# Kernel tuning notes

Hardware: AMD Instinct MI355X
Metric: run time of the kernel (lower is better)

Reference implementation:

```python
import jax, jax.numpy as jnp
import numpy as np

EMBED_DIM = 1024
HEAD_NUM = 16
HEAD_DIM = EMBED_DIM // HEAD_NUM
T, B, S = 2048, 4, 2048


def setup_inputs() -> dict:
    key = jax.random.key(0)
    ks = jax.random.split(key, 11)
    s = 0.02
    return {
        "query": jax.random.normal(ks[0], (T, B, EMBED_DIM), jnp.float32),
        "key": jax.random.normal(ks[1], (S, B, EMBED_DIM), jnp.float32),
        "value": jax.random.normal(ks[2], (S, B, EMBED_DIM), jnp.float32),
        "q_proj_weight": jax.random.normal(ks[3], (EMBED_DIM, EMBED_DIM), jnp.float32) * s,
        "k_proj_weight": jax.random.normal(ks[4], (EMBED_DIM, EMBED_DIM), jnp.float32) * s,
        "v_proj_weight": jax.random.normal(ks[5], (EMBED_DIM, EMBED_DIM), jnp.float32) * s,
        "in_proj_bias": jax.random.normal(ks[6], (3 * EMBED_DIM,), jnp.float32) * s,
        "bias_k": jax.random.normal(ks[7], (1, 1, EMBED_DIM), jnp.float32) * s,
        "bias_v": jax.random.normal(ks[8], (1, 1, EMBED_DIM), jnp.float32) * s,
        "out_proj_weight": jax.random.normal(ks[9], (EMBED_DIM, EMBED_DIM), jnp.float32) * s,
        "out_proj_bias": jax.random.normal(ks[10], (EMBED_DIM,), jnp.float32) * s,
    }


def reference(query, key, value, q_proj_weight, k_proj_weight, v_proj_weight,
              in_proj_bias, bias_k, bias_v, out_proj_weight, out_proj_bias):
    t, b, e = query.shape
    h, hd = HEAD_NUM, HEAD_DIM
    scaling = float(hd) ** -0.5
    # input projections (F.linear: x @ W.T + b)
    q = (query @ q_proj_weight.T + in_proj_bias[:e]) * scaling          # [T,B,E]
    k = key @ k_proj_weight.T + in_proj_bias[e:2 * e]                   # [S,B,E]
    v = value @ v_proj_weight.T + in_proj_bias[2 * e:]                  # [S,B,E]
    # append bias_k / bias_v token along the sequence dim
    k = jnp.concatenate([k, jnp.broadcast_to(bias_k, (1, b, e))], axis=0)  # [S+1,B,E]
    v = jnp.concatenate([v, jnp.broadcast_to(bias_v, (1, b, e))], axis=0)  # [S+1,B,E]
    # split heads: [L, B, E] -> [B*H, L, hd]
    q = q.reshape(t, b * h, hd).transpose(1, 0, 2)
    k = k.reshape(-1, b * h, hd).transpose(1, 0, 2)
    v = v.reshape(-1, b * h, hd).transpose(1, 0, 2)
    # full O(T*S) attention, as in the original bmm->softmax->bmm
    weights = jax.nn.softmax(jnp.einsum('nqd,nkd->nqk', q, k), axis=-1)  # [B*H,T,S+1]
    out = jnp.einsum('nqk,nkd->nqd', weights, v)                         # [B*H,T,hd]
    out = out.transpose(1, 0, 2).reshape(t, b, e)
    out = out @ out_proj_weight.T + out_proj_bias
    avg_weights = weights.sum(axis=1) / h                                # [B*H,S+1]
    return out, avg_weights
```

## Files before the change

### kernel.cpp

```cpp
#include <hip/hip_runtime.h>

#define T_DIM 2048
#define B_DIM 4
#define S_DIM 2048
#define E_DIM 1024
#define H_NUM 16
#define HD    64
#define NH    64
#define SP1   2049
#define SPAD  2112
#define NCHUNK 33

typedef short bf16x8 __attribute__((ext_vector_type(8)));
typedef short bf16x4 __attribute__((ext_vector_type(4)));
typedef float f32x4  __attribute__((ext_vector_type(4)));
typedef float f32x16 __attribute__((ext_vector_type(16)));
typedef unsigned int u32;

#define QSCALE 0.18033688011112042f

#if __has_builtin(__builtin_amdgcn_exp2f)
__device__ __forceinline__ float exp2_fast(float x) { return __builtin_amdgcn_exp2f(x); }
#else
__device__ __forceinline__ float exp2_fast(float x) { return __expf(x * 0.6931471805599453f); }
#endif

__device__ __forceinline__ unsigned short f2bf(float x) {
    union { float f; unsigned int u; } v; v.f = x;
    unsigned int r = v.u + 0x7FFFu + ((v.u >> 16) & 1u);
    return (unsigned short)(r >> 16);
}

__device__ __forceinline__ u32 cvtpk_bf16(float lo, float hi) {
    u32 r;
    asm("v_cvt_pk_bf16_f32 %0, %1, %2" : "=v"(r) : "v"(lo), "v"(hi));
    return r;
}
__device__ __forceinline__ void plswap(u32& a, u32& b) {
    asm("v_permlane32_swap_b32 %0, %1" : "+v"(a), "+v"(b));
}

__global__ __launch_bounds__(256)
void cvt_w4(const float* __restrict__ w0, const float* __restrict__ w1,
            const float* __restrict__ w2, const float* __restrict__ w3,
            short* __restrict__ dst)
{
    const int y = blockIdx.y;
    const float* src = (y == 0) ? w0 : (y == 1) ? w1 : (y == 2) ? w2 : w3;
    short* d = dst + (size_t)y * E_DIM * E_DIM;
    const int i = blockIdx.x * 256 + threadIdx.x;
    const float4* s = reinterpret_cast<const float4*>(src) + (size_t)i * 2;
    float4 a = s[0], b = s[1];
    uint4 o;
    o.x = cvtpk_bf16(a.x, a.y); o.y = cvtpk_bf16(a.z, a.w);
    o.z = cvtpk_bf16(b.x, b.y); o.w = cvtpk_bf16(b.z, b.w);
    *(reinterpret_cast<uint4*>(d) + i) = o;
}

template<int MODE>
__global__ __launch_bounds__(256)
void gemm_bf16(const void* __restrict__ Xq, const void* __restrict__ Xk,
               const void* __restrict__ Xv, const short* __restrict__ Wall,
               const float* __restrict__ biasAll, void* __restrict__ outp)
{
    __shared__ short As[128][72];
    __shared__ short Bs[128][72];
    const int bm = blockIdx.x, bn = blockIdx.y;
    const int z = (MODE == 0) ? blockIdx.z : 0;
    const void* Ap = (MODE == 3) ? Xq : (z == 0) ? Xq : (z == 1) ? Xk : Xv;
    const short* W = Wall + (size_t)z * E_DIM * E_DIM;
    const float* bias = biasAll + z * E_DIM;

    const int tid = threadIdx.x;
    const int l = tid & 63, w = tid >> 6;
    const int wr = w >> 1, wc = w & 1;
    const int lr = l & 15, lg = l >> 4;
    const int rb = tid >> 3, cg = tid & 7;

    float4 paA[4], paB[4];
    bf16x8 pa3[4];
    bf16x8 pb[4];

    auto load_tiles = [&](int k0) {
#pragma unroll
        for (int it = 0; it < 4; ++it) {
            const int row = it * 32 + rb;
            if (MODE == 3) {
                const int m = bm * 128 + row;
                const size_t asrc =
                    ((size_t)((m & 3) * 16 + (k0 >> 6)) * T_DIM + (m >> 2)) * HD + cg * 8;
                pa3[it] = *reinterpret_cast<const bf16x8*>((const short*)Ap + asrc);
            } else {
                const float* ap = (const float*)Ap + (size_t)(bm * 128 + row) * E_DIM + k0 + cg * 8;
                paA[it] = *reinterpret_cast<const float4*>(ap);
                paB[it] = *reinterpret_cast<const float4*>(ap + 4);
            }
            pb[it] = *reinterpret_cast<const bf16x8*>(
                W + (size_t)(bn * 128 + row) * E_DIM + k0 + cg * 8);
        }
    };
    auto write_tiles = [&]() {
#pragma unroll
        for (int it = 0; it < 4; ++it) {
            const int row = it * 32 + rb;
            if (MODE == 3) {
                *reinterpret_cast<bf16x8*>(&As[row][cg * 8]) = pa3[it];
            } else {
                uint4 st;
                st.x = cvtpk_bf16(paA[it].x, paA[it].y); st.y = cvtpk_bf16(paA[it].z, paA[it].w);
                st.z = cvtpk_bf16(paB[it].x, paB[it].y); st.w = cvtpk_bf16(paB[it].z, paB[it].w);
                *reinterpret_cast<uint4*>(&As[row][cg * 8]) = st;
            }
            *reinterpret_cast<bf16x8*>(&Bs[row][cg * 8]) = pb[it];
        }
    };

    load_tiles(0);
    write_tiles();
    __syncthreads();

    f32x4 acc[4][4] = {};

    for (int k0 = 0; k0 < E_DIM; k0 += 64) {
        const bool more = (k0 + 64 < E_DIM);
        if (more) load_tiles(k0 + 64);

        __builtin_amdgcn_s_setprio(1);
#pragma unroll
        for (int c = 0; c < 2; ++c) {
            bf16x8 af[4], bf[4];
#pragma unroll
            for (int mi = 0; mi < 4; ++mi)
                af[mi] = *reinterpret_cast<const bf16x8*>(&As[wr * 64 + mi * 16 + lr][c * 32 + lg * 8]);
#pragma unroll
            for (int ni = 0; ni < 4; ++ni)
                bf[ni] = *reinterpret_cast<const bf16x8*>(&Bs[wc * 64 + ni * 16 + lr][c * 32 + lg * 8]);
#pragma unroll
            for (int mi = 0; mi < 4; ++mi)
#pragma unroll
                for (int ni = 0; ni < 4; ++ni)
                    acc[mi][ni] = __builtin_amdgcn_mfma_f32_16x16x32_bf16(
                        af[mi], bf[ni], acc[mi][ni], 0, 0, 0);
        }
        __builtin_amdgcn_s_setprio(0);

        if (more) {
            __syncthreads();
            write_tiles();
            __syncthreads();
        }
    }

#pragma unroll
    for (int mi = 0; mi < 4; ++mi)
#pragma unroll
        for (int ni = 0; ni < 4; ++ni) {
            const int colg = bn * 128 + wc * 64 + ni * 16 + lr;
            const float bv = bias[colg];
#pragma unroll
            for (int r = 0; r < 4; ++r) {
                const int m = bm * 128 + wr * 64 + mi * 16 + lg * 4 + r;
                float v = acc[mi][ni][r] + bv;
                if (MODE == 3) {
                    ((float*)outp)[(size_t)m * E_DIM + colg] = v;
                } else {
                    if (z == 0) v *= QSCALE;
                    const int seq = m >> 2, b = m & 3;
                    const int head = colg >> 6, d = colg & 63;
                    const int sd = (z == 0) ? T_DIM : SPAD;
                    short* ob = (short*)outp;
                    if (z == 1) ob += (size_t)NH * T_DIM * HD;
                    else if (z == 2) ob += (size_t)NH * T_DIM * HD + (size_t)NH * SPAD * HD;
                    ob[((size_t)(b * 16 + head) * sd + seq) * HD + d] = (short)f2bf(v);
                }
            }
        }
}

__global__ void fill_kv_pad(short* __restrict__ k_h, short* __restrict__ v_h,
                            const float* __restrict__ bias_k,
                            const float* __restrict__ bias_v)
{
    const int d   = threadIdx.x;
    const int row = S_DIM + blockIdx.x;
    const int n   = blockIdx.y;
    short bk = 0, bv = 0;
    if (row == S_DIM) {
        bk = (short)f2bf(bias_k[(n & 15) * HD + d]);
        bv = (short)f2bf(bias_v[(n & 15) * HD + d]);
    }
    const size_t idx = ((size_t)n * SPAD + row) * HD + d;
    k_h[idx] = bk;
    v_h[idx] = bv;
}

__global__ __launch_bounds__(512, 4)
void attn_mfma(const short* __restrict__ q_h, const short* __restrict__ k_h,
               const short* __restrict__ v_h, short* __restrict__ o_h,
               float* __restrict__ m_arr, float* __restrict__ l_arr)
{
    __shared__ short KsD[2][64 * 64];
    __shared__ short VtD[2][64 * 64];

    const int id = blockIdx.x;
    const int xcd = id & 7, slot = id >> 3;
    const int n = xcd * 8 + (slot >> 3);
    const int q0 = (slot & 7) * 256;

    const int tid = threadIdx.x, l = tid & 63, w = tid >> 6;
    const int ql = l & 31;
    const int hi = l >> 5;
    const int qrow = q0 + w * 32 + ql;

    const int krow = tid >> 3, kcg = tid & 7;
    const int kswz = (kcg * 16) ^ ((krow & 7) << 4);
    const int sp = tid & 31, dq = tid >> 5;

    const short* kbase = k_h + (size_t)n * SPAD * HD;
    const short* vbase = v_h + (size_t)n * SPAD * HD;

    bf16x8 aq0, aq1, aq2, aq3;
    {
        const short* qp = q_h + ((size_t)n * T_DIM + qrow) * HD + hi * 8;
        aq0 = *(const bf16x8*)(qp);
        aq1 = *(const bf16x8*)(qp + 16);
        aq2 = *(const bf16x8*)(qp + 32);
        aq3 = *(const bf16x8*)(qp + 48);
    }

    bf16x8 pk  = *(const bf16x8*)(kbase + (size_t)krow * HD + kcg * 8);
    bf16x4 pva = *(const bf16x4*)(vbase + (size_t)(2 * sp) * HD + dq * 4);
    bf16x4 pvb = *(const bf16x4*)(vbase + (size_t)(2 * sp + 1) * HD + dq * 4);
    {
        char* KsB = (char*)KsD[0];
        char* VtB = (char*)VtD[0];
        *(bf16x8*)(KsB + krow * 128 + kswz) = pk;
#pragma unroll
        for (int j = 0; j < 4; ++j) {
            u32 pkd = (u32)(unsigned short)pva[j] | ((u32)(unsigned short)pvb[j] << 16);
            const int d = dq * 4 + j;
            *(u32*)(VtB + d * 128 + ((4 * sp) ^ ((d & 7) << 4))) = pkd;
        }
    }
    __syncthreads();

    float m_run = -1e30f, l_run = 0.f;
    f32x16 accA, accB;
#pragma unroll
    for (int r = 0; r < 16; ++r) { accA[r] = 0.f; accB[r] = 0.f; }

    for (int kc = 0; kc < NCHUNK; ++kc) {
        const char* KsB = (const char*)KsD[kc & 1];
        const char* VtB = (const char*)VtD[kc & 1];
        const bool more = (kc + 1 < NCHUNK);

        if (more) {
            const int s0n = (kc + 1) * 64;
            pk  = *(const bf16x8*)(kbase + (size_t)(s0n + krow) * HD + kcg * 8);
            pva = *(const bf16x4*)(vbase + (size_t)(s0n + 2 * sp) * HD + dq * 4);
            pvb = *(const bf16x4*)(vbase + (size_t)(s0n + 2 * sp + 1) * HD + dq * 4);
        }

        f32x16 sc0, sc1;
#pragma unroll
        for (int r = 0; r < 16; ++r) { sc0[r] = 0.f; sc1[r] = 0.f; }
        __builtin_amdgcn_s_setprio(1);
#pragma unroll
        for (int sl = 0; sl < 4; ++sl) {
            const int cb = ((sl * 32) + hi * 16) ^ ((ql & 7) << 4);
            bf16x8 kf0 = *(const bf16x8*)(KsB + ql * 128 + cb);
            bf16x8 kf1 = *(const bf16x8*)(KsB + (32 + ql) * 128 + cb);
            bf16x8 qf = (sl == 0) ? aq0 : (sl == 1) ? aq1 : (sl == 2) ? aq2 : aq3;
            sc0 = __builtin_amdgcn_mfma_f32_32x32x16_bf16(kf0, qf, sc0, 0, 0, 0);
            sc1 = __builtin_amdgcn_mfma_f32_32x32x16_bf16(kf1, qf, sc1, 0, 0, 0);
        }
        __builtin_amdgcn_s_setprio(0);

        const int s0 = kc * 64;
        if (s0 + 64 > SP1) {
#pragma unroll
            for (int r = 0; r < 16; ++r) {
                const int key = (r & 3) + 8 * (r >> 2) + 4 * hi;
                if (s0 + key >= SP1)      sc0[r] = -1e30f;
                if (s0 + 32 + key >= SP1) sc1[r] = -1e30f;
            }
        }

        float mv[16];
#pragma unroll
        for (int r = 0; r < 16; ++r) mv[r] = fmaxf(sc0[r], sc1[r]);
#pragma unroll
        for (int s = 8; s > 0; s >>= 1)
#pragma unroll
            for (int r = 0; r < s; ++r) mv[r] = fmaxf(mv[r], mv[r + s]);
        float mx = fmaxf(mv[0], __shfl_xor(mv[0], 32));
        if (!__all(mx - m_run <= 8.0f)) {
            const float mnew = fmaxf(m_run, mx);
            const float fac = exp2_fast(m_run - mnew);
            l_run *= fac;
#pragma unroll
            for (int r = 0; r < 16; ++r) { accA[r] *= fac; accB[r] *= fac; }
            m_run = mnew;
        }
        float p0[16], p1[16];
#pragma unroll
        for (int r = 0; r < 16; ++r) p0[r] = exp2_fast(sc0[r] - m_run);
#pragma unroll
        for (int r = 0; r < 16; ++r) p1[r] = exp2_fast(sc1[r] - m_run);
        float sv[16];
#pragma unroll
        for (int r = 0; r < 16; ++r) sv[r] = p0[r] + p1[r];
#pragma unroll
        for (int s = 8; s > 0; s >>= 1)
#pragma unroll
            for (int r = 0; r < s; ++r) sv[r] += sv[r + s];
        l_run += sv[0] + __shfl_xor(sv[0], 32);

        union PF { u32 u[4]; bf16x8 v; };
        PF pf0, pf1, pf2, pf3;
        {
            u32 a0 = cvtpk_bf16(p0[0], p0[1]),   b0 = cvtpk_bf16(p0[4], p0[5]);   plswap(a0, b0);
            u32 a1 = cvtpk_bf16(p0[2], p0[3]),   b1 = cvtpk_bf16(p0[6], p0[7]);   plswap(a1, b1);
            u32 a2 = cvtpk_bf16(p0[8], p0[9]),   b2 = cvtpk_bf16(p0[12], p0[13]); plswap(a2, b2);
            u32 a3 = cvtpk_bf16(p0[10], p0[11]), b3 = cvtpk_bf16(p0[14], p0[15]); plswap(a3, b3);
            pf0.u[0] = a0; pf0.u[1] = a1; pf0.u[2] = b0; pf0.u[3] = b1;
            pf1.u[0] = a2; pf1.u[1] = a3; pf1.u[2] = b2; pf1.u[3] = b3;
            u32 c0 = cvtpk_bf16(p1[0], p1[1]),   d0_ = cvtpk_bf16(p1[4], p1[5]);   plswap(c0, d0_);
            u32 c1 = cvtpk_bf16(p1[2], p1[3]),   d1_ = cvtpk_bf16(p1[6], p1[7]);   plswap(c1, d1_);
            u32 c2 = cvtpk_bf16(p1[8], p1[9]),   d2_ = cvtpk_bf16(p1[12], p1[13]); plswap(c2, d2_);
            u32 c3 = cvtpk_bf16(p1[10], p1[11]), d3_ = cvtpk_bf16(p1[14], p1[15]); plswap(c3, d3_);
            pf2.u[0] = c0; pf2.u[1] = c1; pf2.u[2] = d0_; pf2.u[3] = d1_;
            pf3.u[0] = c2; pf3.u[1] = c3; pf3.u[2] = d2_; pf3.u[3] = d3_;
        }

        __builtin_amdgcn_s_setprio(1);
#pragma unroll
        for (int ksl = 0; ksl < 4; ++ksl) {
            const int cb = ((ksl * 32) + hi * 16) ^ ((ql & 7) << 4);
            bf16x8 vf0 = *(const bf16x8*)(VtB + ql * 128 + cb);
            bf16x8 vf1 = *(const bf16x8*)(VtB + (32 + ql) * 128 + cb);
            const bf16x8 pv = (ksl == 0) ? pf0.v : (ksl == 1) ? pf1.v : (ksl == 2) ? pf2.v : pf3.v;
            accA = __builtin_amdgcn_mfma_f32_32x32x16_bf16(vf0, pv, accA, 0, 0, 0);
            accB = __builtin_amdgcn_mfma_f32_32x32x16_bf16(vf1, pv, accB, 0, 0, 0);
        }
        __builtin_amdgcn_s_setprio(0);

        if (more) {
            char* KsN = (char*)KsD[(kc & 1) ^ 1];
            char* VtN = (char*)VtD[(kc & 1) ^ 1];
            *(bf16x8*)(KsN + krow * 128 + kswz) = pk;
#pragma unroll
            for (int j = 0; j < 4; ++j) {
                u32 pkd = (u32)(unsigned short)pva[j] | ((u32)(unsigned short)pvb[j] << 16);
                const int d = dq * 4 + j;
                *(u32*)(VtN + d * 128 + ((4 * sp) ^ ((d & 7) << 4))) = pkd;
            }
            __syncthreads();
        }
    }

    const float il = 1.0f / l_run;
    short* orow = o_h + ((size_t)n * T_DIM + qrow) * HD;
#pragma unroll
    for (int rq = 0; rq < 4; ++rq) {
        uint2 st;
        st.x = cvtpk_bf16(accA[rq * 4 + 0] * il, accA[rq * 4 + 1] * il);
        st.y = cvtpk_bf16(accA[rq * 4 + 2] * il, accA[rq * 4 + 3] * il);
        *(uint2*)(orow + rq * 8 + hi * 4) = st;
        uint2 st2;
        st2.x = cvtpk_bf16(accB[rq * 4 + 0] * il, accB[rq * 4 + 1] * il);
        st2.y = cvtpk_bf16(accB[rq * 4 + 2] * il, accB[rq * 4 + 3] * il);
        *(uint2*)(orow + 32 + rq * 8 + hi * 4) = st2;
    }
    if (hi == 0) {
        m_arr[n * T_DIM + qrow] = m_run;
        l_arr[n * T_DIM + qrow] = l_run;
    }
}

__global__ __launch_bounds__(256)
void colsum_mfma(const short* __restrict__ q_h, const short* __restrict__ k_h,
                 const float* __restrict__ m_arr, const float* __restrict__ l_arr,
                 float* __restrict__ avg_out)
{
    __shared__ short Qs[2][64][72];
    __shared__ float msh[2][64];
    __shared__ float lih[2][64];

    const int id = blockIdx.x;
    const int xcd = id & 7, slot = id >> 3;
    const int n = xcd * 8 + slot / 33;
    const int s0 = (slot % 33) * 64;

    const int tid = threadIdx.x, l = tid & 63, w = tid >> 6;
    const int lr = l & 15, lg = l >> 4;
    const int qr = tid >> 3, qcg = tid & 7;

    const short* qbase = q_h + (size_t)n * T_DIM * HD;

    bf16x8 ak[2];
#pragma unroll
    for (int c = 0; c < 2; ++c)
        ak[c] = *reinterpret_cast<const bf16x8*>(
            k_h + ((size_t)n * SPAD + s0 + w * 16 + lr) * HD + c * 32 + lg * 8);

    bf16x8 qa = *(const bf16x8*)(qbase + (size_t)qr * HD + qcg * 8);
    bf16x8 qb = *(const bf16x8*)(qbase + (size_t)(32 + qr) * HD + qcg * 8);
    float mlv = 0.f;
    if (tid < 64) mlv = m_arr[n * T_DIM + tid];
    else if (tid < 128) mlv = l_arr[n * T_DIM + tid - 64];
    *(bf16x8*)&Qs[0][qr][qcg * 8] = qa;
    *(bf16x8*)&Qs[0][32 + qr][qcg * 8] = qb;
    if (tid < 64) msh[0][tid] = mlv;
    else if (tid < 128) lih[0][tid - 64] = 1.0f / mlv;
    __syncthreads();

    float csum[4] = {0.f, 0.f, 0.f, 0.f};

    for (int it = 0; it < T_DIM / 64; ++it) {
        const int buf = it & 1;
        const bool more = (it + 1 < T_DIM / 64);
        if (more) {
            const int qo = (it + 1) * 64;
            qa = *(const bf16x8*)(qbase + (size_t)(qo + qr) * HD + qcg * 8);
            qb = *(const bf16x8*)(qbase + (size_t)(qo + 32 + qr) * HD + qcg * 8);
            if (tid < 64) mlv = m_arr[n * T_DIM + qo + tid];
            else if (tid < 128) mlv = l_arr[n * T_DIM + qo + tid - 64];
        }
        __builtin_amdgcn_s_setprio(1);
#pragma unroll
        for (int qt = 0; qt < 4; ++qt) {
            bf16x8 bq0 = *reinterpret_cast<const bf16x8*>(&Qs[buf][qt * 16 + lr][lg * 8]);
            bf16x8 bq1 = *reinterpret_cast<const bf16x8*>(&Qs[buf][qt * 16 + lr][32 + lg * 8]);
            f32x4 z = {0.f, 0.f, 0.f, 0.f};
            z = __builtin_amdgcn_mfma_f32_16x16x32_bf16(ak[0], bq0, z, 0, 0, 0);
            z = __builtin_amdgcn_mfma_f32_16x16x32_bf16(ak[1], bq1, z, 0, 0, 0);
            const float mq = msh[buf][qt * 16 + lr];
            const float lq = lih[buf][qt * 16 + lr];
#pragma unroll
            for (int r = 0; r < 4; ++r)
                csum[r] += exp2_fast(z[r] - mq) * lq;
        }
        __builtin_amdgcn_s_setprio(0);
        if (more) {
            *(bf16x8*)&Qs[buf ^ 1][qr][qcg * 8] = qa;
            *(bf16x8*)&Qs[buf ^ 1][32 + qr][qcg * 8] = qb;
            if (tid < 64) msh[buf ^ 1][tid] = mlv;
            else if (tid < 128) lih[buf ^ 1][tid - 64] = 1.0f / mlv;
            __syncthreads();
        }
    }

#pragma unroll
    for (int r = 0; r < 4; ++r) {
        float v = csum[r];
        v += __shfl_xor(v, 1, 16);
        v += __shfl_xor(v, 2, 16);
        v += __shfl_xor(v, 4, 16);
        v += __shfl_xor(v, 8, 16);
        if (lr == 0) {
            const int key = s0 + w * 16 + lg * 4 + r;
            if (key < SP1) avg_out[(size_t)n * SP1 + key] = v * 0.0625f;
        }
    }
}

extern "C" void kernel_launch(void* const* d_in, const int* in_sizes, int n_in,
                              void* d_out, int out_size, void* d_ws, size_t ws_size,
                              hipStream_t stream)
{
    const float* query   = (const float*)d_in[0];
    const float* key     = (const float*)d_in[1];
    const float* value   = (const float*)d_in[2];
    const float* wq      = (const float*)d_in[3];
    const float* wk      = (const float*)d_in[4];
    const float* wv      = (const float*)d_in[5];
    const float* in_bias = (const float*)d_in[6];
    const float* bias_k  = (const float*)d_in[7];
    const float* bias_v  = (const float*)d_in[8];
    const float* wo      = (const float*)d_in[9];
    const float* out_b   = (const float*)d_in[10];
    float* out = (float*)d_out;

    short* wqb = (short*)d_ws;
    short* wob = wqb + (size_t)3 * E_DIM * E_DIM;
    short* q_h = wqb + (size_t)4 * E_DIM * E_DIM;
    short* k_h = q_h + (size_t)NH * T_DIM * HD;
    short* v_h = k_h + (size_t)NH * SPAD * HD;
    short* o_h = v_h + (size_t)NH * SPAD * HD;
    float* m_arr = (float*)(o_h + (size_t)NH * T_DIM * HD);
    float* l_arr = m_arr + (size_t)NH * T_DIM;

    const dim3 blk(256);
    hipLaunchKernelGGL(cvt_w4, dim3(512, 4), blk, 0, stream, wq, wk, wv, wo, wqb);

    hipLaunchKernelGGL((gemm_bf16<0>), dim3(64, 8, 3), blk, 0, stream,
                       (const void*)query, (const void*)key, (const void*)value,
                       wqb, in_bias, (void*)q_h);
    hipLaunchKernelGGL(fill_kv_pad, dim3(SPAD - S_DIM, NH), dim3(64), 0, stream,
                       k_h, v_h, bias_k, bias_v);
    hipLaunchKernelGGL(attn_mfma, dim3(512), dim3(512), 0, stream,
                       q_h, k_h, v_h, o_h, m_arr, l_arr);
    hipLaunchKernelGGL(colsum_mfma, dim3(2112), blk, 0, stream,
                       q_h, k_h, m_arr, l_arr, out + (size_t)T_DIM * B_DIM * E_DIM);
    hipLaunchKernelGGL((gemm_bf16<3>), dim3(64, 8), blk, 0, stream,
                       (const void*)o_h, (const void*)o_h, (const void*)o_h,
                       wob, out_b, (void*)out);
}
```

Baseline: 294.1 us.

## Pre-convert QKV inputs to bf16 and stage GEMM tiles via direct global-to-LDS loads

Adds a separate kernel that converts query/key/value from fp32 to bf16 into workspace, so the projection GEMM reads bf16 only. The GEMM now loads tiles with global_load_lds straight into unpadded LDS instead of going through registers. This drops the register prefetch double-buffering, removes the row padding, and sets launch bounds to 4 blocks per CU. It costs an extra full pass over the activations, leaves no overlap between loads and MFMA, and unpadded LDS rows may cause bank conflicts on fragment reads.

```diff
diff --git a/kernel.cpp b/kernel.cpp
--- a/kernel.cpp
+++ b/kernel.cpp
@@ -10,6 +10,7 @@
 #define SP1   2049
 #define SPAD  2112
 #define NCHUNK 33
+#define NTOKE ((size_t)T_DIM * B_DIM * E_DIM)
 
 typedef short bf16x8 __attribute__((ext_vector_type(8)));
 typedef short bf16x4 __attribute__((ext_vector_type(4)));
@@ -38,6 +39,12 @@
 }
 __device__ __forceinline__ void plswap(u32& a, u32& b) {
     asm("v_permlane32_swap_b32 %0, %1" : "+v"(a), "+v"(b));
+}
+
+__device__ __forceinline__ void load_lds16(const void* g, void* l) {
+    __builtin_amdgcn_global_load_lds(
+        (const __attribute__((address_space(1))) unsigned int*)g,
+        (__attribute__((address_space(3))) unsigned int*)l, 16, 0, 0);
 }
 
 __global__ __launch_bounds__(256)
@@ -57,73 +64,58 @@
     *(reinterpret_cast<uint4*>(d) + i) = o;
 }
 
+__global__ __launch_bounds__(256)
+void cvt_in(const float* __restrict__ q, const float* __restrict__ k,
+            const float* __restrict__ v, short* __restrict__ dst)
+{
+    const int y = blockIdx.y;
+    const float* src = (y == 0) ? q : (y == 1) ? k : v;
+    short* d = dst + (size_t)y * NTOKE;
+    const size_t i = (size_t)blockIdx.x * 256 + threadIdx.x;
+    const float4* s = reinterpret_cast<const float4*>(src) + i * 2;
+    float4 a = s[0], b = s[1];
+    uint4 o;
+    o.x = cvtpk_bf16(a.x, a.y); o.y = cvtpk_bf16(a.z, a.w);
+    o.z = cvtpk_bf16(b.x, b.y); o.w = cvtpk_bf16(b.z, b.w);
+    *(reinterpret_cast<uint4*>(d) + i) = o;
+}
+
 template<int MODE>
-__global__ __launch_bounds__(256)
-void gemm_bf16(const void* __restrict__ Xq, const void* __restrict__ Xk,
-               const void* __restrict__ Xv, const short* __restrict__ Wall,
+__global__ __launch_bounds__(256, 4)
+void gemm_bf16(const short* __restrict__ Abase, const short* __restrict__ Wall,
                const float* __restrict__ biasAll, void* __restrict__ outp)
 {
-    __shared__ short As[128][72];
-    __shared__ short Bs[128][72];
+    __shared__ short As[128][64];
+    __shared__ short Bs[128][64];
     const int bm = blockIdx.x, bn = blockIdx.y;
     const int z = (MODE == 0) ? blockIdx.z : 0;
-    const void* Ap = (MODE == 3) ? Xq : (z == 0) ? Xq : (z == 1) ? Xk : Xv;
-    const short* W = Wall + (size_t)z * E_DIM * E_DIM;
+    const short* Az = Abase + (MODE == 0 ? (size_t)z * NTOKE : 0);
+    const short* W  = Wall + (size_t)z * E_DIM * E_DIM;
     const float* bias = biasAll + z * E_DIM;
 
     const int tid = threadIdx.x;
     const int l = tid & 63, w = tid >> 6;
     const int wr = w >> 1, wc = w & 1;
     const int lr = l & 15, lg = l >> 4;
-    const int rb = tid >> 3, cg = tid & 7;
-
-    float4 paA[4], paB[4];
-    bf16x8 pa3[4];
-    bf16x8 pb[4];
-
-    auto load_tiles = [&](int k0) {
-#pragma unroll
-        for (int it = 0; it < 4; ++it) {
-            const int row = it * 32 + rb;
+    const int srow = tid >> 3, scol = (tid & 7) * 8;
+
+    f32x4 acc[4][4] = {};
+
+    for (int k0 = 0; k0 < E_DIM; k0 += 64) {
+#pragma unroll
+        for (int r = 0; r < 4; ++r) {
+            const int row = r * 32 + srow;
+            const short* ga;
             if (MODE == 3) {
                 const int m = bm * 128 + row;
-                const size_t asrc =
-                    ((size_t)((m & 3) * 16 + (k0 >> 6)) * T_DIM + (m >> 2)) * HD + cg * 8;
-                pa3[it] = *reinterpret_cast<const bf16x8*>((const short*)Ap + asrc);
+                ga = Az + ((size_t)((m & 3) * 16 + (k0 >> 6)) * T_DIM + (m >> 2)) * HD + scol;
             } else {
-                const float* ap = (const float*)Ap + (size_t)(bm * 128 + row) * E_DIM + k0 + cg * 8;
-                paA[it] = *reinterpret_cast<const float4*>(ap);
-                paB[it] = *reinterpret_cast<const float4*>(ap + 4);
+                ga = Az + (size_t)(bm * 128 + row) * E_DIM + k0 + scol;
             }
-            pb[it] = *reinterpret_cast<const bf16x8*>(
-                W + (size_t)(bn * 128 + row) * E_DIM + k0 + cg * 8);
-        }
-    };
-    auto write_tiles = [&]() {
-#pragma unroll
-        for (int it = 0; it < 4; ++it) {
-            const int row = it * 32 + rb;
-            if (MODE == 3) {
-                *reinterpret_cast<bf16x8*>(&As[row][cg * 8]) = pa3[it];
-            } else {
-                uint4 st;
-                st.x = cvtpk_bf16(paA[it].x, paA[it].y); st.y = cvtpk_bf16(paA[it].z, paA[it].w);
-                st.z = cvtpk_bf16(paB[it].x, paB[it].y); st.w = cvtpk_bf16(paB[it].z, paB[it].w);
-                *reinterpret_cast<uint4*>(&As[row][cg * 8]) = st;
-            }
-            *reinterpret_cast<bf16x8*>(&Bs[row][cg * 8]) = pb[it];
-        }
-    };
-
-    load_tiles(0);
-    write_tiles();
-    __syncthreads();
-
-    f32x4 acc[4][4] = {};
-
-    for (int k0 = 0; k0 < E_DIM; k0 += 64) {
-        const bool more = (k0 + 64 < E_DIM);
-        if (more) load_tiles(k0 + 64);
+            load_lds16(ga, &As[row][scol]);
+            load_lds16(W + (size_t)(bn * 128 + row) * E_DIM + k0 + scol, &Bs[row][scol]);
+        }
+        __syncthreads();
 
         __builtin_amdgcn_s_setprio(1);
 #pragma unroll
@@ -143,12 +135,7 @@
                         af[mi], bf[ni], acc[mi][ni], 0, 0, 0);
         }
         __builtin_amdgcn_s_setprio(0);
-
-        if (more) {
-            __syncthreads();
-            write_tiles();
-            __syncthreads();
-        }
+        __syncthreads();
     }
 
 #pragma unroll
@@ -482,9 +469,10 @@
     const float* out_b   = (const float*)d_in[10];
     float* out = (float*)d_out;
 
-    short* wqb = (short*)d_ws;
-    short* wob = wqb + (size_t)3 * E_DIM * E_DIM;
-    short* q_h = wqb + (size_t)4 * E_DIM * E_DIM;
+    short* wqb    = (short*)d_ws;
+    short* wob    = wqb + (size_t)3 * E_DIM * E_DIM;
+    short* qkv_bf = wqb + (size_t)4 * E_DIM * E_DIM;
+    short* q_h = qkv_bf + 3 * NTOKE;
     short* k_h = q_h + (size_t)NH * T_DIM * HD;
     short* v_h = k_h + (size_t)NH * SPAD * HD;
     short* o_h = v_h + (size_t)NH * SPAD * HD;
@@ -493,10 +481,10 @@
 
     const dim3 blk(256);
     hipLaunchKernelGGL(cvt_w4, dim3(512, 4), blk, 0, stream, wq, wk, wv, wo, wqb);
+    hipLaunchKernelGGL(cvt_in, dim3(4096, 3), blk, 0, stream, query, key, value, qkv_bf);
 
     hipLaunchKernelGGL((gemm_bf16<0>), dim3(64, 8, 3), blk, 0, stream,
-                       (const void*)query, (const void*)key, (const void*)value,
-                       wqb, in_bias, (void*)q_h);
+                       qkv_bf, wqb, in_bias, (void*)q_h);
     hipLaunchKernelGGL(fill_kv_pad, dim3(SPAD - S_DIM, NH), dim3(64), 0, stream,
                        k_h, v_h, bias_k, bias_v);
     hipLaunchKernelGGL(attn_mfma, dim3(512), dim3(512), 0, stream,
@@ -504,6 +492,5 @@
     hipLaunchKernelGGL(colsum_mfma, dim3(2112), blk, 0, stream,
                        q_h, k_h, m_arr, l_arr, out + (size_t)T_DIM * B_DIM * E_DIM);
     hipLaunchKernelGGL((gemm_bf16<3>), dim3(64, 8), blk, 0, stream,
-                       (const void*)o_h, (const void*)o_h, (const void*)o_h,
-                       wob, out_b, (void*)out);
-}
+                       o_h, wob, out_b, (void*)out);
+}
```

After: 289.5 us. No clear change (-1.5%).
